# Performance work log

Measured on AMD Instinct MI355X. Metric: run time of the kernel, lower is better.

## Reference

```python
import jax, jax.numpy as jnp
import numpy as np
from jax import lax

N, S, K, V, C, D, NH, NB, HD = 4, 1024, 4, 32000, 1000, 512, 8, 6, 2048
DH = D // NH
CAP = round((S // K) * 1.0)  # expert capacity = Seq//K * capacity_factor


def setup_inputs() -> dict:
    key = jax.random.key(0)
    ks = jax.random.split(key, 12)
    nrm = lambda k, shape: jax.random.normal(k, shape, dtype=jnp.float32) * 0.02
    return dict(
        x_in=jax.random.randint(ks[0], (N, S), 0, V),
        y_target=jax.random.randint(ks[1], (N, S), 0, C),
        tok_emb=nrm(ks[2], (K, V, D)),
        pos_emb=nrm(ks[3], (K, S, D)),
        ln1_s=jnp.ones((K, NB, D)), ln1_b=jnp.zeros((K, NB, D)),
        Wqkv=nrm(ks[4], (K, NB, D, 3 * D)), bqkv=jnp.zeros((K, NB, 3 * D)),
        Wo=nrm(ks[5], (K, NB, D, D)), bo=jnp.zeros((K, NB, D)),
        ln2_s=jnp.ones((K, NB, D)), ln2_b=jnp.zeros((K, NB, D)),
        W1=nrm(ks[6], (K, NB, D, HD)), b1=jnp.zeros((K, NB, HD)),
        W2=nrm(ks[7], (K, NB, HD, D)), b2=jnp.zeros((K, NB, D)),
        lnf_s=jnp.ones((K, D)), lnf_b=jnp.zeros((K, D)),
        Wcls=nrm(ks[8], (K, D, C)), bcls=jnp.zeros((K, C)),
        Wconf=nrm(ks[9], (K, D, 1)), bconf=jnp.zeros((K, 1)),
    )


def _ln(x, s, b):
    m = x.mean(-1, keepdims=True)
    v = jnp.var(x, axis=-1, keepdims=True)
    return (x - m) * lax.rsqrt(v + 1e-5) * s + b


def reference(x_in, y_target, tok_emb, pos_emb, ln1_s, ln1_b, Wqkv, bqkv, Wo, bo,
              ln2_s, ln2_b, W1, b1, W2, b2, lnf_s, lnf_b, Wcls, bcls, Wconf, bconf):
    causal = jnp.tril(jnp.ones((S, S), dtype=bool))

    def model_fwd(te, pe, l1s, l1b, wqkv, bq, wo, bo_, l2s, l2b, w1, b1_, w2, b2_, lfs, lfb, wc, bc, wcf, bcf):
        x = te[x_in] + pe[None]  # [N,S,D]
        for i in range(NB):
            h = _ln(x, l1s[i], l1b[i])
            qkv = h @ wqkv[i] + bq[i]
            q, k, v = jnp.split(qkv, 3, axis=-1)
            q = q.reshape(N, S, NH, DH); k = k.reshape(N, S, NH, DH); v = v.reshape(N, S, NH, DH)
            att = jnp.einsum('nqhd,nkhd->nhqk', q, k) / np.float32(np.sqrt(DH))
            att = jax.nn.softmax(jnp.where(causal, att, jnp.float32(-1e9)), axis=-1)
            o = jnp.einsum('nhqk,nkhd->nqhd', att, v).reshape(N, S, D)
            x = x + o @ wo[i] + bo_[i]
            h = _ln(x, l2s[i], l2b[i])
            x = x + jax.nn.gelu(h @ w1[i] + b1_[i]) @ w2[i] + b2_[i]
        x = _ln(x, lfs, lfb)
        return x @ wc + bc, x @ wcf + bcf  # logits [N,S,C], confidence [N,S,1]

    clf, conf = jax.vmap(model_fwd)(tok_emb, pos_emb, ln1_s, ln1_b, Wqkv, bqkv, Wo, bo,
                                    ln2_s, ln2_b, W1, b1, W2, b2, lnf_s, lnf_b, Wcls, bcls, Wconf, bconf)
    combined_classifier = jnp.transpose(clf, (1, 0, 2, 3))       # [N,K,S,C]
    combined_confidence = jnp.transpose(conf[..., 0], (1, 0, 2))  # [N,K,S]

    # --- capacity-constrained auction routing on detached logits ---
    logp = jax.nn.log_softmax(lax.stop_gradient(combined_classifier), axis=-1)
    tgt = jnp.broadcast_to(y_target[:, None, :, None], (N, K, S, 1))
    loss = -jnp.take_along_axis(logp, tgt, axis=-1)[..., 0]  # per-token CE, [N,K,S]
    order = jnp.argsort(loss, axis=1, stable=True)            # [N,K,S] models sorted by loss
    order_s = jnp.transpose(order, (2, 0, 1))                 # [S,N,K]
    rows = jnp.arange(N)

    def step(tc, chunk):  # tc: token_count [N,K]; chunk: [N,K]
        tcm = jnp.take_along_axis(tc, chunk, axis=1)
        best = jnp.argmax((tcm < CAP).astype(jnp.float32), axis=1)
        chosen = chunk[rows, best]
        return tc.at[rows, chosen].add(1.0), chosen

    _, chosen = lax.scan(step, jnp.zeros((N, K), dtype=jnp.float32), order_s)
    activated_models_indices = chosen.T  # [N,S]

    mask = jax.nn.one_hot(activated_models_indices, K, dtype=combined_classifier.dtype)  # [N,S,K]
    mask = jnp.transpose(mask, (0, 2, 1))[..., None]  # [N,K,S,1]
    out = (combined_classifier * mask).sum(axis=1)    # [N,S,C]
    return out, combined_confidence, activated_models_indices
```

## Files before the change

kernel.cpp:

```cpp
#include <hip/hip_runtime.h>
#include <hip/hip_bf16.h>

#define N_  4
#define S_  1024
#define K_  4
#define V_  32000
#define C_  1000
#define D_  512
#define NH_ 8
#define NB_ 6
#define HD_ 2048
#define DH_ 64
#define CAP_ 256
#define M_  (N_*S_)

typedef __attribute__((ext_vector_type(8))) short short8_t;
typedef __attribute__((ext_vector_type(4))) float f32x4_t;

#define MFMA16(a,b,c) __builtin_amdgcn_mfma_f32_16x16x32_bf16((a),(b),(c),0,0,0)

#define HSPLANE ((size_t)M_ * D_)
#define WTMAX   ((size_t)524288)

static __device__ __forceinline__ float bfround(float v) {
    unsigned u = __float_as_uint(v);
    u = (u + 0x7FFFu + ((u >> 16) & 1u)) & 0xFFFF0000u;
    return __uint_as_float(u);
}
static __device__ __forceinline__ void split3(float v, unsigned short& a, unsigned short& b, unsigned short& c) {
    const float f0 = bfround(v);      const float r1 = v - f0;
    const float f1 = bfround(r1);     const float f2 = bfround(r1 - f1);
    a = (unsigned short)(__float_as_uint(f0) >> 16);
    b = (unsigned short)(__float_as_uint(f1) >> 16);
    c = (unsigned short)(__float_as_uint(f2) >> 16);
}
static __device__ __forceinline__ float b2f(unsigned short u) {
    return __uint_as_float((unsigned)u << 16);
}

__global__ __launch_bounds__(256) void embed_kernel(const int* __restrict__ x_in,
    const float* __restrict__ tok, const float* __restrict__ pos, float* __restrict__ x)
{
    const int idx = blockIdx.x * 256 + threadIdx.x;
    const int total = M_ * (D_ / 4);
    if (idx >= total) return;
    const int d = (idx & (D_ / 4 - 1)) * 4;
    const int row = idx >> 7;
    const int s = row & (S_ - 1);
    const int t = x_in[row];
    const float4 a = *(const float4*)(tok + (size_t)t * D_ + d);
    const float4 b = *(const float4*)(pos + (size_t)s * D_ + d);
    float4 r; r.x = a.x + b.x; r.y = a.y + b.y; r.z = a.z + b.z; r.w = a.w + b.w;
    *(float4*)(x + (size_t)row * D_ + d) = r;
}

__global__ __launch_bounds__(256) void ln_kernel(const float* __restrict__ x,
    const float* __restrict__ sc, const float* __restrict__ bi, unsigned short* __restrict__ hs)
{
    const int row = blockIdx.x, tid = threadIdx.x;
    const float* xr = x + (size_t)row * D_;
    float v0 = xr[tid], v1 = xr[tid + 256];
    float s1 = v0 + v1;
#pragma unroll
    for (int off = 32; off; off >>= 1) s1 += __shfl_down(s1, off, 64);
    __shared__ float red[8];
    __shared__ float stat[2];
    const int wid = tid >> 6, lane = tid & 63;
    if (lane == 0) red[wid] = s1;
    __syncthreads();
    if (tid == 0) stat[0] = (red[0] + red[1] + red[2] + red[3]) * (1.f / (float)D_);
    __syncthreads();
    const float mean = stat[0];
    const float d0 = v0 - mean, d1 = v1 - mean;
    float s2 = d0 * d0 + d1 * d1;
#pragma unroll
    for (int off = 32; off; off >>= 1) s2 += __shfl_down(s2, off, 64);
    if (lane == 0) red[wid] = s2;
    __syncthreads();
    if (tid == 0) stat[1] = (red[0] + red[1] + red[2] + red[3]) * (1.f / (float)D_);
    __syncthreads();
    const float rstd = rsqrtf(stat[1] + 1e-5f);
    const float o0 = d0 * rstd * sc[tid] + bi[tid];
    const float o1 = d1 * rstd * sc[tid + 256] + bi[tid + 256];
    unsigned short a, b, c;
    const size_t base = (size_t)row * D_ + tid;
    split3(o0, a, b, c);
    hs[base] = a; hs[base + HSPLANE] = b; hs[base + 2 * HSPLANE] = c;
    split3(o1, a, b, c);
    hs[base + 256] = a; hs[base + 256 + HSPLANE] = b; hs[base + 256 + 2 * HSPLANE] = c;
}

__global__ __launch_bounds__(256) void wsplit_kernel(const float* __restrict__ W, int ldw, int NcTrue,
    unsigned short* __restrict__ Wt, size_t bplane, int Kd)
{
    const int tid = threadIdx.x;
    const int n = blockIdx.x * 64 + (tid & 63);
    const int k0 = blockIdx.y * 32 + (tid >> 6) * 8;
    unsigned short q0[8], q1[8], q2[8];
    if (n < NcTrue) {
#pragma unroll
        for (int j = 0; j < 8; ++j) split3(W[(size_t)(k0 + j) * ldw + n], q0[j], q1[j], q2[j]);
    } else {
#pragma unroll
        for (int j = 0; j < 8; ++j) { q0[j] = 0; q1[j] = 0; q2[j] = 0; }
    }
    unsigned short* dst = Wt + (size_t)n * Kd + k0;
    *(uint4*)dst = *(uint4*)&q0[0];
    *(uint4*)(dst + bplane) = *(uint4*)&q1[0];
    *(uint4*)(dst + 2 * bplane) = *(uint4*)&q2[0];
}

template<int EPI>
__global__ __launch_bounds__(256) void gemm64(const unsigned short* __restrict__ A3, size_t aplane,
    const unsigned short* __restrict__ Bt, size_t bplane, const float* __restrict__ bias,
    void* __restrict__ Cv, size_t cplane, int Nc, int Kd, int lda, int ldc)
{
    __shared__ __align__(16) unsigned short Bs[3][64][40];
    const int tid = threadIdx.x;
    const int bm = blockIdx.y * 128, bn = blockIdx.x * 64;
    const int wid = tid >> 6, lane = tid & 63;
    const int wm = (wid >> 1) * 64, wn = (wid & 1) * 32;
    const int lr = lane & 15, lg = lane >> 4;
    const int scol = tid >> 2, skq = tid & 3;
    const unsigned short* Bp0 = Bt + (size_t)(bn + scol) * Kd + skq * 8;

    f32x4_t acc[4][2] = {};

    for (int k0 = 0; k0 < Kd; k0 += 32) {
        const uint4 bq0 = *(const uint4*)(Bp0 + k0);
        const uint4 bq1 = *(const uint4*)(Bp0 + bplane + k0);
        const uint4 bq2 = *(const uint4*)(Bp0 + 2 * bplane + k0);
        short8_t af[3][4];
#pragma unroll
        for (int m = 0; m < 4; ++m) {
            const unsigned short* ap = A3 + (size_t)(bm + wm + m * 16 + lr) * lda + k0 + lg * 8;
            af[0][m] = *(const short8_t*)ap;
            af[1][m] = *(const short8_t*)(ap + aplane);
            af[2][m] = *(const short8_t*)(ap + 2 * aplane);
        }
        __syncthreads();
        *(uint4*)&Bs[0][scol][skq * 8] = bq0;
        *(uint4*)&Bs[1][scol][skq * 8] = bq1;
        *(uint4*)&Bs[2][scol][skq * 8] = bq2;
        __syncthreads();
        short8_t bg[3][2];
#pragma unroll
        for (int s = 0; s < 3; ++s)
#pragma unroll
            for (int n2 = 0; n2 < 2; ++n2)
                bg[s][n2] = *(const short8_t*)&Bs[s][wn + n2 * 16 + lr][lg * 8];
#pragma unroll
        for (int m = 0; m < 4; ++m)
#pragma unroll
            for (int n2 = 0; n2 < 2; ++n2) {
                f32x4_t c = acc[m][n2];
                c = MFMA16(af[0][m], bg[0][n2], c);
                c = MFMA16(af[0][m], bg[1][n2], c);
                c = MFMA16(af[1][m], bg[0][n2], c);
                c = MFMA16(af[1][m], bg[1][n2], c);
                c = MFMA16(af[0][m], bg[2][n2], c);
                c = MFMA16(af[2][m], bg[0][n2], c);
                acc[m][n2] = c;
            }
    }
#pragma unroll
    for (int m = 0; m < 4; ++m)
#pragma unroll
        for (int n2 = 0; n2 < 2; ++n2) {
            const int col = bn + wn + n2 * 16 + lr;
            if (col >= Nc) continue;
            const float bv = bias ? bias[col] : 0.f;
            const int row0 = bm + wm + m * 16 + lg * 4;
#pragma unroll
            for (int r = 0; r < 4; ++r) {
                float v = acc[m][n2][r] + bv;
                if (EPI == 2) {
                    const float t = v;
                    const float g = 0.5f * t * (1.f + tanhf(0.7978845608028654f * (t + 0.044715f * t * t * t)));
                    unsigned short a, b, c;
                    split3(g, a, b, c);
                    unsigned short* Cp = (unsigned short*)Cv + (size_t)(row0 + r) * ldc + col;
                    Cp[0] = a; Cp[cplane] = b; Cp[2 * cplane] = c;
                } else {
                    float* cp = (float*)Cv + (size_t)(row0 + r) * ldc + col;
                    if (EPI == 1) v += *cp;
                    *cp = v;
                }
            }
        }
}

__global__ __launch_bounds__(256) void rerun_kernel(const unsigned short* __restrict__ A,
    const unsigned short* __restrict__ B0, const float* __restrict__ bias,
    const int* __restrict__ chosen, const int kk, float* __restrict__ out)
{
    __shared__ int anyrow;
    const int tid = threadIdx.x;
    const int bm = blockIdx.y * 128, bn = blockIdx.x * 64;
    if (tid == 0) anyrow = 0;
    __syncthreads();
    if (tid < 128 && chosen[bm + tid] == kk) anyrow = 1;
    __syncthreads();
    if (!anyrow) return;
    const int wid = tid >> 6, lane = tid & 63;
    const int wm = (wid >> 1) * 64, wn = (wid & 1) * 32;
    const int lr = lane & 15, lg = lane >> 4;
    f32x4_t acc[4][2] = {};
    for (int k0 = 0; k0 < D_; k0 += 32) {
        short8_t af[4], bg[2];
#pragma unroll
        for (int m = 0; m < 4; ++m)
            af[m] = *(const short8_t*)(A + (size_t)(bm + wm + m * 16 + lr) * D_ + k0 + lg * 8);
#pragma unroll
        for (int n2 = 0; n2 < 2; ++n2)
            bg[n2] = *(const short8_t*)(B0 + (size_t)(bn + wn + n2 * 16 + lr) * D_ + k0 + lg * 8);
#pragma unroll
        for (int m = 0; m < 4; ++m)
#pragma unroll
            for (int n2 = 0; n2 < 2; ++n2)
                acc[m][n2] = MFMA16(af[m], bg[n2], acc[m][n2]);
    }
#pragma unroll
    for (int m = 0; m < 4; ++m)
#pragma unroll
        for (int n2 = 0; n2 < 2; ++n2) {
            const int col = bn + wn + n2 * 16 + lr;
            if (col >= C_) continue;
            const float bv = bias[col];
            const int row0 = bm + wm + m * 16 + lg * 4;
#pragma unroll
            for (int r = 0; r < 4; ++r) {
                const int row = row0 + r;
                if (chosen[row] == kk) out[(size_t)row * C_ + col] = acc[m][n2][r] + bv;
            }
        }
}

__global__ __launch_bounds__(256) void attn_mfma_kernel(const float* __restrict__ qkv, unsigned short* __restrict__ hsO)
{
    __shared__ __align__(16) unsigned short Ks[3][32][72];
    __shared__ __align__(16) unsigned short Vt[3][64][40];
    __shared__ __align__(16) unsigned short Ps[4][3][16][40];
    const int qt = blockIdx.x, hh = blockIdx.y, n = blockIdx.z;
    const int tid = threadIdx.x;
    const int w = tid >> 6, lane = tid & 63;
    const int lr = lane & 15, lg = lane >> 4;
    const size_t rs = 3 * D_;
    const float* base = qkv + (size_t)n * S_ * rs + hh * DH_;

    short8_t qf[3][2];
    {
        const int qrow = qt * 64 + w * 16 + lr;
#pragma unroll
        for (int ks = 0; ks < 2; ++ks) {
            const float* qp = base + (size_t)qrow * rs + ks * 32 + lg * 8;
            float v[8];
            *(float4*)&v[0] = ((const float4*)qp)[0];
            *(float4*)&v[4] = ((const float4*)qp)[1];
#pragma unroll
            for (int j = 0; j < 8; ++j) {
                unsigned short a, b, c;
                split3(v[j], a, b, c);
                qf[0][ks][j] = (short)a; qf[1][ks][j] = (short)b; qf[2][ks][j] = (short)c;
            }
        }
    }

    f32x4_t oacc[4] = {};
    float m_r[4], l_r[4];
#pragma unroll
    for (int r = 0; r < 4; ++r) { m_r[r] = -1e30f; l_r[r] = 0.f; }

    const int ktmax = 2 * qt + 2;
    for (int kt = 0; kt < ktmax; ++kt) {
        __syncthreads();
        {
            const int key = tid & 31, seg = tid >> 5;
            const float* kp = base + (size_t)(kt * 32 + key) * rs + D_ + seg * 8;
            const float* vp = kp + D_;
            float kv[8], vv[8];
            *(float4*)&kv[0] = ((const float4*)kp)[0];
            *(float4*)&kv[4] = ((const float4*)kp)[1];
            *(float4*)&vv[0] = ((const float4*)vp)[0];
            *(float4*)&vv[4] = ((const float4*)vp)[1];
            unsigned short k0a[8], k1a[8], k2a[8];
#pragma unroll
            for (int j = 0; j < 8; ++j) split3(kv[j], k0a[j], k1a[j], k2a[j]);
            *(uint4*)&Ks[0][key][seg * 8] = *(uint4*)&k0a[0];
            *(uint4*)&Ks[1][key][seg * 8] = *(uint4*)&k1a[0];
            *(uint4*)&Ks[2][key][seg * 8] = *(uint4*)&k2a[0];
#pragma unroll
            for (int j = 0; j < 8; ++j) {
                unsigned short a, b, c;
                split3(vv[j], a, b, c);
                Vt[0][seg * 8 + j][key] = a;
                Vt[1][seg * 8 + j][key] = b;
                Vt[2][seg * 8 + j][key] = c;
            }
        }
        __syncthreads();
        f32x4_t sacc[2] = {};
#pragma unroll
        for (int n2 = 0; n2 < 2; ++n2) {
#pragma unroll
            for (int ks = 0; ks < 2; ++ks) {
                short8_t kb0 = *(const short8_t*)&Ks[0][n2 * 16 + lr][ks * 32 + lg * 8];
                short8_t kb1 = *(const short8_t*)&Ks[1][n2 * 16 + lr][ks * 32 + lg * 8];
                short8_t kb2 = *(const short8_t*)&Ks[2][n2 * 16 + lr][ks * 32 + lg * 8];
                f32x4_t c = sacc[n2];
                c = MFMA16(qf[0][ks], kb0, c);
                c = MFMA16(qf[0][ks], kb1, c);
                c = MFMA16(qf[1][ks], kb0, c);
                c = MFMA16(qf[1][ks], kb1, c);
                c = MFMA16(qf[0][ks], kb2, c);
                c = MFMA16(qf[2][ks], kb0, c);
                sacc[n2] = c;
            }
        }
        float p[2][4];
#pragma unroll
        for (int n2 = 0; n2 < 2; ++n2)
#pragma unroll
            for (int r = 0; r < 4; ++r) {
                float s = sacc[n2][r] * 0.125f;
                const int key = kt * 32 + n2 * 16 + lr;
                const int qrow = qt * 64 + w * 16 + lg * 4 + r;
                if (key > qrow) s = -1e30f;
                p[n2][r] = s;
            }
        float scl[4];
#pragma unroll
        for (int r = 0; r < 4; ++r) {
            float tm = fmaxf(p[0][r], p[1][r]);
            tm = fmaxf(tm, __shfl_xor(tm, 1));
            tm = fmaxf(tm, __shfl_xor(tm, 2));
            tm = fmaxf(tm, __shfl_xor(tm, 4));
            tm = fmaxf(tm, __shfl_xor(tm, 8));
            const float mnew = fmaxf(m_r[r], tm);
            scl[r] = expf(m_r[r] - mnew);
            m_r[r] = mnew;
        }
#pragma unroll
        for (int r = 0; r < 4; ++r) {
            p[0][r] = expf(p[0][r] - m_r[r]);
            p[1][r] = expf(p[1][r] - m_r[r]);
            float ts = p[0][r] + p[1][r];
            ts += __shfl_xor(ts, 1);
            ts += __shfl_xor(ts, 2);
            ts += __shfl_xor(ts, 4);
            ts += __shfl_xor(ts, 8);
            l_r[r] = l_r[r] * scl[r] + ts;
        }
#pragma unroll
        for (int nf = 0; nf < 4; ++nf)
#pragma unroll
            for (int r = 0; r < 4; ++r) oacc[nf][r] *= scl[r];
#pragma unroll
        for (int n2 = 0; n2 < 2; ++n2)
#pragma unroll
            for (int r = 0; r < 4; ++r) {
                unsigned short a, b, c;
                split3(p[n2][r], a, b, c);
                Ps[w][0][lg * 4 + r][n2 * 16 + lr] = a;
                Ps[w][1][lg * 4 + r][n2 * 16 + lr] = b;
                Ps[w][2][lg * 4 + r][n2 * 16 + lr] = c;
            }
        short8_t pa0 = *(const short8_t*)&Ps[w][0][lr][lg * 8];
        short8_t pa1 = *(const short8_t*)&Ps[w][1][lr][lg * 8];
        short8_t pa2 = *(const short8_t*)&Ps[w][2][lr][lg * 8];
#pragma unroll
        for (int nf = 0; nf < 4; ++nf) {
            short8_t vb0 = *(const short8_t*)&Vt[0][nf * 16 + lr][lg * 8];
            short8_t vb1 = *(const short8_t*)&Vt[1][nf * 16 + lr][lg * 8];
            short8_t vb2 = *(const short8_t*)&Vt[2][nf * 16 + lr][lg * 8];
            f32x4_t c = oacc[nf];
            c = MFMA16(pa0, vb0, c);
            c = MFMA16(pa0, vb1, c);
            c = MFMA16(pa1, vb0, c);
            c = MFMA16(pa1, vb1, c);
            c = MFMA16(pa0, vb2, c);
            c = MFMA16(pa2, vb0, c);
            oacc[nf] = c;
        }
    }
    float inv[4];
#pragma unroll
    for (int r = 0; r < 4; ++r) inv[r] = 1.f / l_r[r];
#pragma unroll
    for (int nf = 0; nf < 4; ++nf)
#pragma unroll
        for (int r = 0; r < 4; ++r) {
            const int qrow = qt * 64 + w * 16 + lg * 4 + r;
            const size_t idx = ((size_t)n * S_ + qrow) * D_ + hh * DH_ + nf * 16 + lr;
            unsigned short a, b, c;
            split3(oacc[nf][r] * inv[r], a, b, c);
            hsO[idx] = a; hsO[idx + HSPLANE] = b; hsO[idx + 2 * HSPLANE] = c;
        }
}

__global__ __launch_bounds__(256) void conf_kernel(const unsigned short* __restrict__ hs,
    const float* __restrict__ w, const float* __restrict__ bc, float* __restrict__ conf_out, int k)
{
    const int wid = threadIdx.x >> 6, lane = threadIdx.x & 63;
    const int row = blockIdx.x * 4 + wid;
    const unsigned short* h0 = hs + (size_t)row * D_;
    const unsigned short* h1 = h0 + HSPLANE;
    float sm = 0.f;
#pragma unroll
    for (int j = 0; j < 8; ++j) {
        const int i = lane + 64 * j;
        sm += (b2f(h0[i]) + b2f(h1[i])) * w[i];
    }
#pragma unroll
    for (int off = 32; off; off >>= 1) sm += __shfl_down(sm, off, 64);
    if (lane == 0) {
        const int n = row >> 10, s = row & (S_ - 1);
        conf_out[((size_t)n * K_ + k) * S_ + s] = sm + bc[0];
    }
}

__global__ __launch_bounds__(256) void loss_kernel(const float* __restrict__ logits,
    const int* __restrict__ y, float* __restrict__ loss)
{
    const int row = blockIdx.x;
    const float* lr = logits + (size_t)row * C_;
    const int tid = threadIdx.x;
    __shared__ float red[256];
    float mx = -1e30f;
    for (int c = tid; c < C_; c += 256) mx = fmaxf(mx, lr[c]);
    red[tid] = mx; __syncthreads();
    for (int st = 128; st > 0; st >>= 1) {
        if (tid < st) red[tid] = fmaxf(red[tid], red[tid + st]);
        __syncthreads();
    }
    mx = red[0];
    __syncthreads();
    float sm = 0.f;
    for (int c = tid; c < C_; c += 256) sm += expf(lr[c] - mx);
    red[tid] = sm; __syncthreads();
    for (int st = 128; st > 0; st >>= 1) {
        if (tid < st) red[tid] += red[tid + st];
        __syncthreads();
    }
    if (tid == 0) loss[row] = logf(red[0]) + mx - lr[y[row]];
}

__global__ __launch_bounds__(256) void routing_kernel(const float* __restrict__ loss,
    float* __restrict__ idx_out, int* __restrict__ chosen_buf)
{
    __shared__ float l_s[K_][S_];
    __shared__ unsigned char ord_s[S_];
    const int n = blockIdx.x;
    const int tid = threadIdx.x;
#pragma unroll
    for (int k = 0; k < K_; ++k)
        ((float4*)l_s[k])[tid] = ((const float4*)(loss + (size_t)k * M_ + n * S_))[tid];
    __syncthreads();
    for (int s = tid; s < S_; s += 256) {
        float l[K_];
#pragma unroll
        for (int k = 0; k < K_; ++k) l[k] = l_s[k][s];
        int ord[K_] = {0, 1, 2, 3};
#pragma unroll
        for (int i = 1; i < K_; ++i) {
            const int v = ord[i];
            int j = i;
            while (j > 0 && l[ord[j - 1]] > l[v]) { ord[j] = ord[j - 1]; --j; }
            ord[j] = v;
        }
        ord_s[s] = (unsigned char)(ord[0] | (ord[1] << 2) | (ord[2] << 4) | (ord[3] << 6));
    }
    __syncthreads();
    if (tid == 0) {
        int tc[K_] = {0, 0, 0, 0};
        for (int s = 0; s < S_; ++s) {
            const unsigned b = ord_s[s];
            int ch = b & 3;
#pragma unroll
            for (int j = 0; j < K_; ++j) {
                const int m = (b >> (2 * j)) & 3;
                if (tc[m] < CAP_) { ch = m; break; }
            }
            ++tc[ch];
            chosen_buf[n * S_ + s] = ch;
            idx_out[n * S_ + s] = (float)ch;
        }
    }
}

extern "C" void kernel_launch(void* const* d_in, const int* in_sizes, int n_in,
                              void* d_out, int out_size, void* d_ws, size_t ws_size,
                              hipStream_t stream)
{
    const int*   x_in = (const int*)d_in[0];
    const int*   y    = (const int*)d_in[1];
    const float* tok  = (const float*)d_in[2];
    const float* pos  = (const float*)d_in[3];
    const float* ln1s = (const float*)d_in[4];
    const float* ln1b = (const float*)d_in[5];
    const float* Wqkv = (const float*)d_in[6];
    const float* bqkv = (const float*)d_in[7];
    const float* Wo   = (const float*)d_in[8];
    const float* bo   = (const float*)d_in[9];
    const float* ln2s = (const float*)d_in[10];
    const float* ln2b = (const float*)d_in[11];
    const float* W1   = (const float*)d_in[12];
    const float* b1   = (const float*)d_in[13];
    const float* W2   = (const float*)d_in[14];
    const float* b2   = (const float*)d_in[15];
    const float* lnfs = (const float*)d_in[16];
    const float* lnfb = (const float*)d_in[17];
    const float* Wcls = (const float*)d_in[18];
    const float* bcls = (const float*)d_in[19];
    const float* Wcnf = (const float*)d_in[20];
    const float* bcnf = (const float*)d_in[21];

    if (ws_size < 66142208) return;
    float* R = (float*)d_ws;
    unsigned short* hs   = (unsigned short*)(R + (size_t)M_ * 1536);
    float* x             = (float*)(hs + 3 * HSPLANE);
    unsigned short* hfin = (unsigned short*)(x + (size_t)M_ * D_);
    unsigned short* Wt   = hfin + (size_t)K_ * M_ * D_;
    float* loss          = (float*)(Wt + 3 * WTMAX);
    int*   chosen        = (int*)(loss + (size_t)K_ * M_);
    unsigned short* mids = (unsigned short*)R;
    const size_t midplane = (size_t)M_ * 1024;

    float* out      = (float*)d_out;
    float* conf_out = out + (size_t)M_ * C_;
    float* idx_out  = conf_out + (size_t)N_ * K_ * S_;

    for (int k = 0; k < K_; ++k) {
        embed_kernel<<<(M_ * (D_ / 4) + 255) / 256, 256, 0, stream>>>(
            x_in, tok + (size_t)k * V_ * D_, pos + (size_t)k * S_ * D_, x);
        for (int i = 0; i < NB_; ++i) {
            const size_t ki = (size_t)k * NB_ + i;
            ln_kernel<<<M_, 256, 0, stream>>>(x, ln1s + ki * D_, ln1b + ki * D_, hs);
            for (int c = 0; c < 2; ++c) {
                wsplit_kernel<<<dim3(12, 16), 256, 0, stream>>>(
                    Wqkv + ki * D_ * 3 * D_ + c * 768, 3 * D_, 768, Wt, 768 * 512, D_);
                gemm64<0><<<dim3(12, 32), 256, 0, stream>>>(
                    hs, HSPLANE, Wt, 768 * 512, bqkv + ki * 3 * D_ + c * 768,
                    R + c * 768, 0, 768, D_, D_, 3 * D_);
            }
            attn_mfma_kernel<<<dim3(S_ / 64, NH_, N_), 256, 0, stream>>>(R, hs);
            wsplit_kernel<<<dim3(8, 16), 256, 0, stream>>>(Wo + ki * D_ * D_, D_, D_, Wt, 512 * 512, D_);
            gemm64<1><<<dim3(8, 32), 256, 0, stream>>>(
                hs, HSPLANE, Wt, 512 * 512, bo + ki * D_, x, 0, D_, D_, D_, D_);
            ln_kernel<<<M_, 256, 0, stream>>>(x, ln2s + ki * D_, ln2b + ki * D_, hs);
            for (int c = 0; c < 2; ++c) {
                wsplit_kernel<<<dim3(16, 16), 256, 0, stream>>>(
                    W1 + ki * D_ * HD_ + c * 1024, HD_, 1024, Wt, 1024 * 512, D_);
                gemm64<2><<<dim3(16, 32), 256, 0, stream>>>(
                    hs, HSPLANE, Wt, 1024 * 512, b1 + ki * HD_ + c * 1024,
                    mids, midplane, 1024, D_, D_, 1024);
                wsplit_kernel<<<dim3(8, 32), 256, 0, stream>>>(
                    W2 + ki * HD_ * D_ + (size_t)c * 1024 * D_, D_, D_, Wt, 512 * 1024, 1024);
                gemm64<1><<<dim3(8, 32), 256, 0, stream>>>(
                    mids, midplane, Wt, 512 * 1024, (c == 0) ? (b2 + ki * D_) : nullptr,
                    x, 0, D_, 1024, 1024, D_);
            }
        }
        ln_kernel<<<M_, 256, 0, stream>>>(x, lnfs + (size_t)k * D_, lnfb + (size_t)k * D_, hs);
        hipMemcpyAsync(hfin + (size_t)k * M_ * D_, hs, (size_t)M_ * D_ * 2,
                       hipMemcpyDeviceToDevice, stream);
        wsplit_kernel<<<dim3(16, 16), 256, 0, stream>>>(
            Wcls + (size_t)k * D_ * C_, C_, C_, Wt, 1024 * 512, D_);
        gemm64<0><<<dim3(16, 32), 256, 0, stream>>>(
            hs, HSPLANE, Wt, 1024 * 512, bcls + (size_t)k * C_, R, 0, C_, D_, D_, C_);
        conf_kernel<<<M_ / 4, 256, 0, stream>>>(hs, Wcnf + (size_t)k * D_, bcnf + k, conf_out, k);
        loss_kernel<<<M_, 256, 0, stream>>>(R, y, loss + (size_t)k * M_);
    }
    routing_kernel<<<N_, 256, 0, stream>>>(loss, idx_out, chosen);
    for (int k = 0; k < K_; ++k) {
        wsplit_kernel<<<dim3(16, 16), 256, 0, stream>>>(
            Wcls + (size_t)k * D_ * C_, C_, C_, Wt, 1024 * 512, D_);
        rerun_kernel<<<dim3(16, 32), 256, 0, stream>>>(
            hfin + (size_t)k * M_ * D_, Wt, bcls + (size_t)k * C_, chosen, k, out);
    }
}
```

Measured before the change: 13.85 ms.

## Replace gemm64 with 128x128-tiled GEMM staging A and B in LDS with register prefetch

The GEMM tile grows from 128x64 to 128x128, and the A operand is now staged through shared memory alongside B instead of being read per wave directly from global memory. The next k-slice is loaded into registers while the current slice is being computed. The MFMA sequence is reordered so LDS fragment loads interleave with the split-precision products. The aim is more operand reuse per block, less global traffic and hidden load latency, at the cost of more LDS and registers, fewer blocks per launch, and possibly lower occupancy.

```diff
diff --git a/kernel.cpp b/kernel.cpp
--- a/kernel.cpp
+++ b/kernel.cpp
@@ -111,69 +111,101 @@
 }
 
 template<int EPI>
-__global__ __launch_bounds__(256) void gemm64(const unsigned short* __restrict__ A3, size_t aplane,
+__global__ __launch_bounds__(256) void gemm128(const unsigned short* __restrict__ A3, size_t aplane,
     const unsigned short* __restrict__ Bt, size_t bplane, const float* __restrict__ bias,
     void* __restrict__ Cv, size_t cplane, int Nc, int Kd, int lda, int ldc)
 {
-    __shared__ __align__(16) unsigned short Bs[3][64][40];
+    __shared__ __align__(16) unsigned short As[3][128][40];
+    __shared__ __align__(16) unsigned short Bs[3][128][40];
     const int tid = threadIdx.x;
-    const int bm = blockIdx.y * 128, bn = blockIdx.x * 64;
+    const int bm = blockIdx.y * 128, bn = blockIdx.x * 128;
     const int wid = tid >> 6, lane = tid & 63;
-    const int wm = (wid >> 1) * 64, wn = (wid & 1) * 32;
+    const int wm = (wid >> 1) * 64, wn = (wid & 1) * 64;
     const int lr = lane & 15, lg = lane >> 4;
-    const int scol = tid >> 2, skq = tid & 3;
-    const unsigned short* Bp0 = Bt + (size_t)(bn + scol) * Kd + skq * 8;
-
-    f32x4_t acc[4][2] = {};
+    const int srow = tid >> 1, sof = (tid & 1) * 16;
+
+    const unsigned short* Ap = A3 + (size_t)(bm + srow) * lda + sof;
+    const unsigned short* Bp = Bt + (size_t)(bn + srow) * Kd + sof;
+
+    uint4 aq[3][2], bq[3][2];
+#pragma unroll
+    for (int p = 0; p < 3; ++p) {
+        aq[p][0] = *(const uint4*)(Ap + (size_t)p * aplane);
+        aq[p][1] = *(const uint4*)(Ap + (size_t)p * aplane + 8);
+        bq[p][0] = *(const uint4*)(Bp + (size_t)p * bplane);
+        bq[p][1] = *(const uint4*)(Bp + (size_t)p * bplane + 8);
+    }
+
+    f32x4_t acc[4][4] = {};
 
     for (int k0 = 0; k0 < Kd; k0 += 32) {
-        const uint4 bq0 = *(const uint4*)(Bp0 + k0);
-        const uint4 bq1 = *(const uint4*)(Bp0 + bplane + k0);
-        const uint4 bq2 = *(const uint4*)(Bp0 + 2 * bplane + k0);
-        short8_t af[3][4];
-#pragma unroll
-        for (int m = 0; m < 4; ++m) {
-            const unsigned short* ap = A3 + (size_t)(bm + wm + m * 16 + lr) * lda + k0 + lg * 8;
-            af[0][m] = *(const short8_t*)ap;
-            af[1][m] = *(const short8_t*)(ap + aplane);
-            af[2][m] = *(const short8_t*)(ap + 2 * aplane);
-        }
         __syncthreads();
-        *(uint4*)&Bs[0][scol][skq * 8] = bq0;
-        *(uint4*)&Bs[1][scol][skq * 8] = bq1;
-        *(uint4*)&Bs[2][scol][skq * 8] = bq2;
+#pragma unroll
+        for (int p = 0; p < 3; ++p) {
+            *(uint4*)&As[p][srow][sof]     = aq[p][0];
+            *(uint4*)&As[p][srow][sof + 8] = aq[p][1];
+            *(uint4*)&Bs[p][srow][sof]     = bq[p][0];
+            *(uint4*)&Bs[p][srow][sof + 8] = bq[p][1];
+        }
         __syncthreads();
-        short8_t bg[3][2];
-#pragma unroll
-        for (int s = 0; s < 3; ++s)
-#pragma unroll
-            for (int n2 = 0; n2 < 2; ++n2)
-                bg[s][n2] = *(const short8_t*)&Bs[s][wn + n2 * 16 + lr][lg * 8];
-#pragma unroll
-        for (int m = 0; m < 4; ++m)
-#pragma unroll
-            for (int n2 = 0; n2 < 2; ++n2) {
-                f32x4_t c = acc[m][n2];
-                c = MFMA16(af[0][m], bg[0][n2], c);
-                c = MFMA16(af[0][m], bg[1][n2], c);
-                c = MFMA16(af[1][m], bg[0][n2], c);
-                c = MFMA16(af[1][m], bg[1][n2], c);
-                c = MFMA16(af[0][m], bg[2][n2], c);
-                c = MFMA16(af[2][m], bg[0][n2], c);
-                acc[m][n2] = c;
-            }
+        if (k0 + 32 < Kd) {
+#pragma unroll
+            for (int p = 0; p < 3; ++p) {
+                aq[p][0] = *(const uint4*)(Ap + (size_t)p * aplane + k0 + 32);
+                aq[p][1] = *(const uint4*)(Ap + (size_t)p * aplane + k0 + 40);
+                bq[p][0] = *(const uint4*)(Bp + (size_t)p * bplane + k0 + 32);
+                bq[p][1] = *(const uint4*)(Bp + (size_t)p * bplane + k0 + 40);
+            }
+        }
+        short8_t af0[4], bg0[4], afx[4], bgx[4];
+#pragma unroll
+        for (int m = 0; m < 4; ++m) af0[m] = *(const short8_t*)&As[0][wm + m * 16 + lr][lg * 8];
+#pragma unroll
+        for (int n = 0; n < 4; ++n) bg0[n] = *(const short8_t*)&Bs[0][wn + n * 16 + lr][lg * 8];
+#pragma unroll
+        for (int m = 0; m < 4; ++m)
+#pragma unroll
+            for (int n = 0; n < 4; ++n) acc[m][n] = MFMA16(af0[m], bg0[n], acc[m][n]);
+#pragma unroll
+        for (int n = 0; n < 4; ++n) bgx[n] = *(const short8_t*)&Bs[1][wn + n * 16 + lr][lg * 8];
+#pragma unroll
+        for (int m = 0; m < 4; ++m)
+#pragma unroll
+            for (int n = 0; n < 4; ++n) acc[m][n] = MFMA16(af0[m], bgx[n], acc[m][n]);
+#pragma unroll
+        for (int m = 0; m < 4; ++m) afx[m] = *(const short8_t*)&As[1][wm + m * 16 + lr][lg * 8];
+#pragma unroll
+        for (int m = 0; m < 4; ++m)
+#pragma unroll
+            for (int n = 0; n < 4; ++n) acc[m][n] = MFMA16(afx[m], bg0[n], acc[m][n]);
+#pragma unroll
+        for (int m = 0; m < 4; ++m)
+#pragma unroll
+            for (int n = 0; n < 4; ++n) acc[m][n] = MFMA16(afx[m], bgx[n], acc[m][n]);
+#pragma unroll
+        for (int n = 0; n < 4; ++n) bgx[n] = *(const short8_t*)&Bs[2][wn + n * 16 + lr][lg * 8];
+#pragma unroll
+        for (int m = 0; m < 4; ++m)
+#pragma unroll
+            for (int n = 0; n < 4; ++n) acc[m][n] = MFMA16(af0[m], bgx[n], acc[m][n]);
+#pragma unroll
+        for (int m = 0; m < 4; ++m) afx[m] = *(const short8_t*)&As[2][wm + m * 16 + lr][lg * 8];
+#pragma unroll
+        for (int m = 0; m < 4; ++m)
+#pragma unroll
+            for (int n = 0; n < 4; ++n) acc[m][n] = MFMA16(afx[m], bg0[n], acc[m][n]);
     }
 #pragma unroll
     for (int m = 0; m < 4; ++m)
 #pragma unroll
-        for (int n2 = 0; n2 < 2; ++n2) {
-            const int col = bn + wn + n2 * 16 + lr;
+        for (int n = 0; n < 4; ++n) {
+            const int col = bn + wn + n * 16 + lr;
             if (col >= Nc) continue;
             const float bv = bias ? bias[col] : 0.f;
             const int row0 = bm + wm + m * 16 + lg * 4;
 #pragma unroll
             for (int r = 0; r < 4; ++r) {
-                float v = acc[m][n2][r] + bv;
+                float v = acc[m][n][r] + bv;
                 if (EPI == 2) {
                     const float t = v;
                     const float g = 0.5f * t * (1.f + tanhf(0.7978845608028654f * (t + 0.044715f * t * t * t)));
@@ -539,24 +571,24 @@
             for (int c = 0; c < 2; ++c) {
                 wsplit_kernel<<<dim3(12, 16), 256, 0, stream>>>(
                     Wqkv + ki * D_ * 3 * D_ + c * 768, 3 * D_, 768, Wt, 768 * 512, D_);
-                gemm64<0><<<dim3(12, 32), 256, 0, stream>>>(
+                gemm128<0><<<dim3(6, 32), 256, 0, stream>>>(
                     hs, HSPLANE, Wt, 768 * 512, bqkv + ki * 3 * D_ + c * 768,
                     R + c * 768, 0, 768, D_, D_, 3 * D_);
             }
             attn_mfma_kernel<<<dim3(S_ / 64, NH_, N_), 256, 0, stream>>>(R, hs);
             wsplit_kernel<<<dim3(8, 16), 256, 0, stream>>>(Wo + ki * D_ * D_, D_, D_, Wt, 512 * 512, D_);
-            gemm64<1><<<dim3(8, 32), 256, 0, stream>>>(
+            gemm128<1><<<dim3(4, 32), 256, 0, stream>>>(
                 hs, HSPLANE, Wt, 512 * 512, bo + ki * D_, x, 0, D_, D_, D_, D_);
             ln_kernel<<<M_, 256, 0, stream>>>(x, ln2s + ki * D_, ln2b + ki * D_, hs);
             for (int c = 0; c < 2; ++c) {
                 wsplit_kernel<<<dim3(16, 16), 256, 0, stream>>>(
                     W1 + ki * D_ * HD_ + c * 1024, HD_, 1024, Wt, 1024 * 512, D_);
-                gemm64<2><<<dim3(16, 32), 256, 0, stream>>>(
+                gemm128<2><<<dim3(8, 32), 256, 0, stream>>>(
                     hs, HSPLANE, Wt, 1024 * 512, b1 + ki * HD_ + c * 1024,
                     mids, midplane, 1024, D_, D_, 1024);
                 wsplit_kernel<<<dim3(8, 32), 256, 0, stream>>>(
                     W2 + ki * HD_ * D_ + (size_t)c * 1024 * D_, D_, D_, Wt, 512 * 1024, 1024);
-                gemm64<1><<<dim3(8, 32), 256, 0, stream>>>(
+                gemm128<1><<<dim3(4, 32), 256, 0, stream>>>(
                     mids, midplane, Wt, 512 * 1024, (c == 0) ? (b2 + ki * D_) : nullptr,
                     x, 0, D_, 1024, 1024, D_);
             }
@@ -566,7 +598,7 @@
                        hipMemcpyDeviceToDevice, stream);
         wsplit_kernel<<<dim3(16, 16), 256, 0, stream>>>(
             Wcls + (size_t)k * D_ * C_, C_, C_, Wt, 1024 * 512, D_);
-        gemm64<0><<<dim3(16, 32), 256, 0, stream>>>(
+        gemm128<0><<<dim3(8, 32), 256, 0, stream>>>(
             hs, HSPLANE, Wt, 1024 * 512, bcls + (size_t)k * C_, R, 0, C_, D_, D_, C_);
         conf_kernel<<<M_ / 4, 256, 0, stream>>>(hs, Wcnf + (size_t)k * D_, bcnf + k, conf_out, k);
         loss_kernel<<<M_, 256, 0, stream>>>(R, y, loss + (size_t)k * M_);
```

After: 21.88 ms. 1.58x slower.
